# Performance work log

Hardware: AMD Instinct MI355X
Metric: run time of the kernel (lower is better)

Reference implementation:

```python
import jax, jax.numpy as jnp
import numpy as np

N = 100000   # nodes
E = 625000   # edges
D = 128      # input feature dim
H = 128      # hidden_channels
L = 2        # num_layers
NEG = 0.2    # leaky relu negative slope
BN_EPS = 1e-5


def setup_inputs() -> dict:
    key = jax.random.key(0)
    ks = jax.random.split(key, 12)
    s = 0.05
    return {
        "x": jax.random.normal(ks[0], (N, D), jnp.float32),
        "edge_index": jax.random.randint(ks[1], (2, E), 0, N, dtype=jnp.int32),
        "Wl": jax.random.normal(ks[2], (L, D, H), jnp.float32) * s,   # GATv2 lin_l (source)
        "bl": jax.random.normal(ks[3], (L, H), jnp.float32) * s,
        "Wr": jax.random.normal(ks[4], (L, D, H), jnp.float32) * s,   # GATv2 lin_r (target)
        "br": jax.random.normal(ks[5], (L, H), jnp.float32) * s,
        "att": jax.random.normal(ks[6], (L, H), jnp.float32) * s,     # attention vector a
        "cb": jax.random.normal(ks[7], (L, H), jnp.float32) * s,      # conv output bias
        "Wlin": jax.random.normal(ks[8], (L, H, H), jnp.float32) * s, # extra Linear
        "blin": jax.random.normal(ks[9], (L, H), jnp.float32) * s,
        "gamma": jnp.ones((L, H), jnp.float32),                       # BatchNorm weight
        "beta": jnp.zeros((L, H), jnp.float32),                       # BatchNorm bias
    }


def reference(x, edge_index, Wl, bl, Wr, br, att, cb, Wlin, blin, gamma, beta):
    src, dst = edge_index[0], edge_index[1]
    for i in range(L):
        # GATv2Conv (1 head, no self-loops)
        xs = x @ Wl[i] + bl[i]                 # [N, H] source transform
        xd = x @ Wr[i] + br[i]                 # [N, H] target transform
        e = jax.nn.leaky_relu(xs[src] + xd[dst], NEG)   # [E, H]
        logits = e @ att[i]                    # [E]
        m = jax.ops.segment_max(logits, dst, num_segments=N)
        a = jnp.exp(logits - m[dst])
        denom = jax.ops.segment_sum(a, dst, num_segments=N) + 1e-16
        alpha = a / denom[dst]                 # scatter-softmax over dst
        out = jax.ops.segment_sum(alpha[:, None] * xs[src], dst, num_segments=N) + cb[i]
        # x += lin(x)
        out = out + out @ Wlin[i] + blin[i]
        # BatchNorm1d (training mode: batch stats, biased var)
        mu = out.mean(axis=0)
        var = out.var(axis=0)
        x = (out - mu) * jax.lax.rsqrt(var + BN_EPS) * gamma[i] + beta[i]
        if i < L - 1:
            x = jax.nn.relu(x)
    return x
```

## Files before the change

kernel.cpp:

```cpp
#include <hip/hip_runtime.h>

#define NN 100000
#define NE 625000
#define HD 128

typedef unsigned int u32;
typedef unsigned short u16;
typedef __bf16 bf16x8 __attribute__((ext_vector_type(8)));
typedef float f32x4 __attribute__((ext_vector_type(4)));
typedef float f32x2 __attribute__((ext_vector_type(2)));

__device__ __forceinline__ u16 f2b(float f) {
  u32 u = __float_as_uint(f);
  u32 r = (u + 0x7FFFu + ((u >> 16) & 1u)) >> 16;
  return (u16)r;
}
__device__ __forceinline__ float b2f(u32 u) { return __uint_as_float(u << 16); }

template <int CTRL>
__device__ __forceinline__ float dppadd(float x) {
  int t = __builtin_amdgcn_update_dpp(0, __float_as_int(x), CTRL, 0xf, 0xf, true);
  return x + __int_as_float(t);
}

__global__ void k_prep_w(const float* __restrict__ Wl, const float* __restrict__ Wr,
                         const float* __restrict__ Wlin, u16* __restrict__ Wt) {
  int i = blockIdx.x * blockDim.x + threadIdx.x;
  if (i >= 6 * 16384) return;
  int mat = i >> 14;
  int l = mat / 3, which = mat % 3;
  int rem = i & 16383;
  int hh = rem >> 7, dd = rem & 127;
  const float* src = (which == 0) ? Wl : (which == 1) ? Wr : Wlin;
  float v = src[l * 16384 + dd * 128 + hh];
  if (which == 2 && dd == hh) v += 1.0f;
  Wt[l * (3 * 16384) + which * 16384 + hh * 128 + dd] = f2b(v);
}

__global__ void k_cast_x(const float* __restrict__ x, u16* __restrict__ xb) {
  int i = blockIdx.x * blockDim.x + threadIdx.x;
  if (i >= NN * 32) return;
  float4 v = *(const float4*)(x + i * 4);
  uint2 o;
  o.x = (u32)f2b(v.x) | ((u32)f2b(v.y) << 16);
  o.y = (u32)f2b(v.z) | ((u32)f2b(v.w) << 16);
  *(uint2*)(xb + i * 4) = o;
}

__global__ void k_hist(const int* __restrict__ dst, int* __restrict__ deg) {
  int e = blockIdx.x * blockDim.x + threadIdx.x;
  if (e < NE) atomicAdd(&deg[dst[e]], 1);
}

__global__ void k_alloc(const int* __restrict__ deg, int* __restrict__ row_start,
                        int* __restrict__ cursor) {
  int idx = blockIdx.x * blockDim.x + threadIdx.x;
  int lane = threadIdx.x & 63;
  int v = (idx < NN) ? deg[idx] : 0;
  int incl = v;
  #pragma unroll
  for (int off = 1; off < 64; off <<= 1) {
    int t = __shfl_up(incl, off, 64);
    if (lane >= off) incl += t;
  }
  int total = __shfl(incl, 63, 64);
  int base = 0;
  if (lane == 63) base = atomicAdd(cursor, total);
  base = __shfl(base, 63, 64);
  if (idx < NN) row_start[idx] = base + incl - v;
}

__global__ void k_fill(const int* __restrict__ src, const int* __restrict__ dst,
                       const int* __restrict__ row_start, int* __restrict__ cnt,
                       int* __restrict__ ss) {
  int e = blockIdx.x * blockDim.x + threadIdx.x;
  if (e >= NE) return;
  int d = dst[e];
  int p = row_start[d] + atomicAdd(&cnt[d], 1);
  ss[p] = src[e];
}

__global__ __launch_bounds__(256) void k_gemm4(
    const u16* __restrict__ A, const u16* __restrict__ Bt0, const u16* __restrict__ Bt1,
    const float* __restrict__ bias0, const float* __restrict__ bias1,
    u16* __restrict__ o0, u16* __restrict__ o1,
    const float* __restrict__ bn_sum, const float* __restrict__ bn_sq,
    const float* __restrict__ bn_g, const float* __restrict__ bn_b,
    float* __restrict__ st_sum, float* __restrict__ st_sq, int nB) {
  __shared__ __align__(16) u16 lA[128 * 136];
  __shared__ __align__(16) u16 lB[64 * 136];
  const int tid = threadIdx.x;
  const int m0 = blockIdx.x * 128;
  const int rr = tid >> 4;
  const int seg = tid & 15;

  float mu[8], sc[8], bb[8];
  if (bn_sum) {
    const float invn = 1.0f / 100000.0f;
    #pragma unroll
    for (int j = 0; j < 8; ++j) {
      int c = seg * 8 + j;
      float m = bn_sum[c] * invn;
      float v = fmaxf(bn_sq[c] * invn - m * m, 0.f);
      mu[j] = m;
      sc[j] = rsqrtf(v + 1e-5f) * bn_g[c];
      bb[j] = bn_b[c];
    }
  }
  #pragma unroll
  for (int p = 0; p < 8; ++p) {
    int row = p * 16 + rr;
    int g = m0 + row;
    int gc = (g < NN) ? g : (NN - 1);
    uint4 v = *(const uint4*)(A + gc * HD + seg * 8);
    if (bn_sum) {
      u32 w[4] = {v.x, v.y, v.z, v.w};
      #pragma unroll
      for (int k = 0; k < 4; ++k) {
        float lo = fmaxf((b2f(w[k] & 0xFFFFu) - mu[2 * k]) * sc[2 * k] + bb[2 * k], 0.f);
        float hi = fmaxf((b2f(w[k] >> 16) - mu[2 * k + 1]) * sc[2 * k + 1] + bb[2 * k + 1], 0.f);
        w[k] = (u32)f2b(lo) | ((u32)f2b(hi) << 16);
      }
      v.x = w[0]; v.y = w[1]; v.z = w[2]; v.w = w[3];
    }
    *(uint4*)(lA + row * 136 + seg * 8) = v;
  }
  #pragma unroll
  for (int p = 0; p < 4; ++p) {
    int n = p * 16 + rr;
    uint4 v = *(const uint4*)(Bt0 + n * HD + seg * 8);
    *(uint4*)(lB + n * 136 + seg * 8) = v;
  }
  __syncthreads();

  const int wv = tid >> 6;
  const int lane = tid & 63;
  const int colt = lane & 15;
  const int kq = lane >> 4;
  const int rq = kq * 4;
  bf16x8 af[2][4];
  #pragma unroll
  for (int tile = 0; tile < 2; ++tile)
    #pragma unroll
    for (int s = 0; s < 4; ++s)
      af[tile][s] = *(const bf16x8*)(lA + ((wv * 2 + tile) * 16 + colt) * 136 + s * 32 + kq * 8);

  for (int pass = 0; pass < nB; ++pass) {
    const u16* Bt = pass ? Bt1 : Bt0;
    u16* o = pass ? o1 : o0;
    const float* bias = pass ? bias1 : bias0;
    if (pass == 1) {
      __syncthreads();
      #pragma unroll
      for (int p = 0; p < 4; ++p) {
        int n = p * 16 + rr;
        uint4 v = *(const uint4*)(Bt + n * HD + seg * 8);
        *(uint4*)(lB + n * 136 + seg * 8) = v;
      }
      __syncthreads();
    }
    #pragma unroll
    for (int half = 0; half < 2; ++half) {
      if (half == 1) {
        __syncthreads();
        #pragma unroll
        for (int p = 0; p < 4; ++p) {
          int n = p * 16 + rr;
          uint4 v = *(const uint4*)(Bt + (64 + n) * HD + seg * 8);
          *(uint4*)(lB + n * 136 + seg * 8) = v;
        }
        __syncthreads();
      }
      #pragma unroll
      for (int tt = 0; tt < 4; ++tt) {
        int t = half * 4 + tt;
        bf16x8 bf[4];
        #pragma unroll
        for (int s = 0; s < 4; ++s)
          bf[s] = *(const bf16x8*)(lB + (tt * 16 + colt) * 136 + s * 32 + kq * 8);
        const int c = t * 16 + colt;
        const float bs = bias[c];
        #pragma unroll
        for (int tile = 0; tile < 2; ++tile) {
          f32x4 acc = {0.f, 0.f, 0.f, 0.f};
          #pragma unroll
          for (int s = 0; s < 4; ++s)
            acc = __builtin_amdgcn_mfma_f32_16x16x32_bf16(af[tile][s], bf[s], acc, 0, 0, 0);
          #pragma unroll
          for (int r = 0; r < 4; ++r)
            lA[((wv * 2 + tile) * 16 + rq + r) * 136 + c] = f2b(acc[r] + bs);
        }
      }
    }
    __syncthreads();
    float s8[8], q8[8];
    #pragma unroll
    for (int j = 0; j < 8; ++j) { s8[j] = 0.f; q8[j] = 0.f; }
    #pragma unroll
    for (int i = 0; i < 8; ++i) {
      int row = i * 16 + rr;
      int g = m0 + row;
      if (g < NN) {
        uint4 v = *(const uint4*)(lA + row * 136 + seg * 8);
        *(uint4*)(o + g * HD + seg * 8) = v;
        if (st_sum && pass == 0) {
          u32 w[4] = {v.x, v.y, v.z, v.w};
          #pragma unroll
          for (int k = 0; k < 4; ++k) {
            float lo = b2f(w[k] & 0xFFFFu), hi = b2f(w[k] >> 16);
            s8[2 * k] += lo; q8[2 * k] += lo * lo;
            s8[2 * k + 1] += hi; q8[2 * k + 1] += hi * hi;
          }
        }
      }
    }
    if (st_sum && pass == 0) {
      __syncthreads();
      float* red = (float*)lB;
      #pragma unroll
      for (int j = 0; j < 8; ++j) {
        red[rr * 128 + seg * 8 + j] = s8[j];
        red[2048 + rr * 128 + seg * 8 + j] = q8[j];
      }
      __syncthreads();
      if (tid < 128) {
        float S = 0.f, Q = 0.f;
        #pragma unroll
        for (int u = 0; u < 16; ++u) {
          S += red[u * 128 + tid];
          Q += red[2048 + u * 128 + tid];
        }
        atomicAdd(&st_sum[tid], S);
        atomicAdd(&st_sq[tid], Q);
      }
    }
  }
}

__global__ __launch_bounds__(256) void k_edge4(
    const u16* __restrict__ xs_b, const u16* __restrict__ xd_b,
    const int* __restrict__ row_start, const int* __restrict__ deg,
    const int* __restrict__ ss, const float* __restrict__ att,
    const float* __restrict__ cb, u16* __restrict__ out_b) {
  int dv = blockIdx.x * 4 + (threadIdx.x >> 6);
  if (dv >= NN) return;
  const int lane = threadIdx.x & 63;
  const int cl = lane & 15;
  const int grp = lane >> 4;

  const float L2E = 1.4426950408889634f;
  float4 av0 = *(const float4*)(att + cl * 8);
  float4 av1 = *(const float4*)(att + cl * 8 + 4);
  float al[8] = {av0.x, av0.y, av0.z, av0.w, av1.x, av1.y, av1.z, av1.w};
  f32x2 a6[4], a4[4];
  #pragma unroll
  for (int k = 0; k < 4; ++k) {
    a6[k].x = L2E * 0.6f * al[2 * k];     a6[k].y = L2E * 0.6f * al[2 * k + 1];
    a4[k].x = L2E * 0.4f * al[2 * k];     a4[k].y = L2E * 0.4f * al[2 * k + 1];
  }
  uint4 xdp = *(const uint4*)(xd_b + dv * HD + cl * 8);
  u32 xdw[4] = {xdp.x, xdp.y, xdp.z, xdp.w};
  f32x2 xd4[4];
  #pragma unroll
  for (int k = 0; k < 4; ++k) {
    xd4[k].x = __uint_as_float(xdw[k] << 16);
    xd4[k].y = __uint_as_float(xdw[k] & 0xFFFF0000u);
  }

  const int base = row_start[dv];
  const int n = deg[dv];
  f32x2 acc[4] = {{0.f, 0.f}, {0.f, 0.f}, {0.f, 0.f}, {0.f, 0.f}};
  float wsum = 0.f;

  for (int e0 = 0; e0 < n; e0 += 4) {
    int e = e0 + grp;
    int idx = ss[base + ((e < n) ? e : 0)];
    uint4 p = *(const uint4*)(xs_b + idx * HD + cl * 8);
    u32 pw[4] = {p.x, p.y, p.z, p.w};
    f32x2 xv[4];
    f32x2 qv = {0.f, 0.f};
    #pragma unroll
    for (int k = 0; k < 4; ++k) {
      f32x2 x2;
      x2.x = __uint_as_float(pw[k] << 16);
      x2.y = __uint_as_float(pw[k] & 0xFFFF0000u);
      xv[k] = x2;
      f32x2 t = x2 + xd4[k];
      f32x2 ab = {__builtin_fabsf(t.x), __builtin_fabsf(t.y)};
      qv += a4[k] * ab;
      qv += a6[k] * t;
    }
    float q = qv.x + qv.y;
    q = dppadd<0xB1>(q);
    q = dppadd<0x4E>(q);
    q = dppadd<0x124>(q);
    q = dppadd<0x128>(q);
    float w = (e < n) ? exp2f(q) : 0.f;
    wsum += w;
    #pragma unroll
    for (int k = 0; k < 4; ++k) acc[k] += xv[k] * w;
  }

  #pragma unroll
  for (int k = 0; k < 4; ++k) {
    acc[k].x += __shfl_xor(acc[k].x, 16, 64);
    acc[k].y += __shfl_xor(acc[k].y, 16, 64);
    acc[k].x += __shfl_xor(acc[k].x, 32, 64);
    acc[k].y += __shfl_xor(acc[k].y, 32, 64);
  }
  wsum += __shfl_xor(wsum, 16, 64);
  wsum += __shfl_xor(wsum, 32, 64);

  if (grp == 0) {
    float inv = 1.f / (wsum + 1e-16f);
    float4 cb0 = *(const float4*)(cb + cl * 8);
    float4 cb1 = *(const float4*)(cb + cl * 8 + 4);
    float cbl[8] = {cb0.x, cb0.y, cb0.z, cb0.w, cb1.x, cb1.y, cb1.z, cb1.w};
    u32 ow[4];
    #pragma unroll
    for (int k = 0; k < 4; ++k) {
      float o0 = acc[k].x * inv + cbl[2 * k];
      float o1 = acc[k].y * inv + cbl[2 * k + 1];
      ow[k] = (u32)f2b(o0) | ((u32)f2b(o1) << 16);
    }
    uint4 o;
    o.x = ow[0]; o.y = ow[1]; o.z = ow[2]; o.w = ow[3];
    *(uint4*)(out_b + dv * HD + cl * 8) = o;
  }
}

__global__ void k_bn(const u16* __restrict__ hb, const float* __restrict__ ssum,
                     const float* __restrict__ ssq, const float* __restrict__ gamma,
                     const float* __restrict__ beta, float* __restrict__ fout) {
  int i = blockIdx.x * blockDim.x + threadIdx.x;
  if (i >= NN * 64) return;
  int cp = (i & 63) * 2;
  u32 xp = ((const u32*)hb)[i];
  float v0 = b2f(xp & 0xFFFFu), v1 = b2f(xp >> 16);
  const float invn = 1.0f / 100000.0f;
  float mu0 = ssum[cp] * invn, mu1 = ssum[cp + 1] * invn;
  float va0 = fmaxf(ssq[cp] * invn - mu0 * mu0, 0.f);
  float va1 = fmaxf(ssq[cp + 1] * invn - mu1 * mu1, 0.f);
  float s0 = rsqrtf(va0 + 1e-5f) * gamma[cp];
  float s1 = rsqrtf(va1 + 1e-5f) * gamma[cp + 1];
  float o0 = (v0 - mu0) * s0 + beta[cp];
  float o1 = (v1 - mu1) * s1 + beta[cp + 1];
  int row = i >> 6;
  *(float2*)(fout + row * 128 + cp) = make_float2(o0, o1);
}

extern "C" void kernel_launch(void* const* d_in, const int* in_sizes, int n_in,
                              void* d_out, int out_size, void* d_ws, size_t ws_size,
                              hipStream_t stream) {
  const float* x    = (const float*)d_in[0];
  const int*   ei   = (const int*)d_in[1];
  const float* Wl   = (const float*)d_in[2];
  const float* bl   = (const float*)d_in[3];
  const float* Wr   = (const float*)d_in[4];
  const float* br   = (const float*)d_in[5];
  const float* att  = (const float*)d_in[6];
  const float* cb   = (const float*)d_in[7];
  const float* Wlin = (const float*)d_in[8];
  const float* blin = (const float*)d_in[9];
  const float* gm   = (const float*)d_in[10];
  const float* bt   = (const float*)d_in[11];
  const int* esrc = ei;
  const int* edst = ei + NE;

  u16* xb    = (u16*)d_ws;
  u16* xs_b  = xb + NN * HD;
  u16* xd_b  = xs_b + NN * HD;
  u16* out_b = xd_b + NN * HD;
  u16* Wt    = out_b + NN * HD;
  int* deg       = (int*)(Wt + 6 * 16384);
  int* cnt       = deg + NN;
  int* cursor    = cnt + NN;
  int* row_start = cursor + 1;
  int* srcs      = row_start + NN;
  float* ssum0   = (float*)(srcs + NE);
  float* ssq0    = ssum0 + 128;
  float* ssum1   = ssq0 + 128;
  float* ssq1    = ssum1 + 128;

  hipMemsetAsync(deg, 0, (size_t)(2 * NN + 1) * 4, stream);
  hipMemsetAsync(ssum0, 0, 4 * 128 * 4, stream);
  k_prep_w<<<(6 * 16384 + 255) / 256, 256, 0, stream>>>(Wl, Wr, Wlin, Wt);
  k_cast_x<<<(NN * 32 + 255) / 256, 256, 0, stream>>>(x, xb);
  k_hist<<<(NE + 255) / 256, 256, 0, stream>>>(edst, deg);
  k_alloc<<<(NN + 255) / 256, 256, 0, stream>>>(deg, row_start, cursor);
  k_fill<<<(NE + 255) / 256, 256, 0, stream>>>(esrc, edst, row_start, cnt, srcs);

  const int gg = (NN + 127) / 128;
  const u16* wt0_l = Wt;             const u16* wt0_r = Wt + 16384;     const u16* wt0_lin = Wt + 2 * 16384;
  const u16* wt1_l = Wt + 3 * 16384; const u16* wt1_r = Wt + 4 * 16384; const u16* wt1_lin = Wt + 5 * 16384;

  k_gemm4<<<gg, 256, 0, stream>>>(xb, wt0_l, wt0_r, bl, br, xs_b, xd_b,
                                  nullptr, nullptr, nullptr, nullptr,
                                  nullptr, nullptr, 2);
  k_edge4<<<(NN + 3) / 4, 256, 0, stream>>>(xs_b, xd_b, row_start, deg, srcs,
                                            att, cb, out_b);
  k_gemm4<<<gg, 256, 0, stream>>>(out_b, wt0_lin, nullptr, blin, nullptr,
                                  out_b, nullptr,
                                  nullptr, nullptr, nullptr, nullptr,
                                  ssum0, ssq0, 1);
  k_gemm4<<<gg, 256, 0, stream>>>(out_b, wt1_l, wt1_r, bl + 128, br + 128,
                                  xs_b, xd_b,
                                  ssum0, ssq0, gm, bt,
                                  nullptr, nullptr, 2);
  k_edge4<<<(NN + 3) / 4, 256, 0, stream>>>(xs_b, xd_b, row_start, deg, srcs,
                                            att + 128, cb + 128, out_b);
  k_gemm4<<<gg, 256, 0, stream>>>(out_b, wt1_lin, nullptr, blin + 128, nullptr,
                                  out_b, nullptr,
                                  nullptr, nullptr, nullptr, nullptr,
                                  ssum1, ssq1, 1);
  k_bn<<<(NN * 64 + 255) / 256, 256, 0, stream>>>(out_b, ssum1, ssq1,
                                                  gm + 128, bt + 128, (float*)d_out);
}
```

Measured before the change: 457.4 us.

## Persistent edge kernel with software-pipelined double-buffered neighbor gathers

The edge aggregation kernel becomes a persistent grid-stride kernel with 2048 blocks. Each wavefront loops over many destination nodes and hoists the att/cb loads out of that loop. Within a node, the first 32 neighbors are gathered two chunks ahead of the compute that uses them, so multiple xs row loads are in flight and gather latency is hidden. Index loads read four consecutive entries and select per group, which relies on 32 zero-padded entries after srcs to stay in bounds. The cost is more registers and an unrolled code path, plus more branching.

```diff
diff --git a/kernel.cpp b/kernel.cpp
--- a/kernel.cpp
+++ b/kernel.cpp
@@ -237,16 +237,16 @@
   }
 }
 
-__global__ __launch_bounds__(256) void k_edge4(
+__global__ __launch_bounds__(256) void k_edge5(
     const u16* __restrict__ xs_b, const u16* __restrict__ xd_b,
     const int* __restrict__ row_start, const int* __restrict__ deg,
     const int* __restrict__ ss, const float* __restrict__ att,
     const float* __restrict__ cb, u16* __restrict__ out_b) {
-  int dv = blockIdx.x * 4 + (threadIdx.x >> 6);
-  if (dv >= NN) return;
   const int lane = threadIdx.x & 63;
   const int cl = lane & 15;
   const int grp = lane >> 4;
+  const int nw = gridDim.x * 4;
+  const int wid = blockIdx.x * 4 + (threadIdx.x >> 6);
 
   const float L2E = 1.4426950408889634f;
   float4 av0 = *(const float4*)(att + cl * 8);
@@ -258,74 +258,105 @@
     a6[k].x = L2E * 0.6f * al[2 * k];     a6[k].y = L2E * 0.6f * al[2 * k + 1];
     a4[k].x = L2E * 0.4f * al[2 * k];     a4[k].y = L2E * 0.4f * al[2 * k + 1];
   }
-  uint4 xdp = *(const uint4*)(xd_b + dv * HD + cl * 8);
-  u32 xdw[4] = {xdp.x, xdp.y, xdp.z, xdp.w};
-  f32x2 xd4[4];
-  #pragma unroll
-  for (int k = 0; k < 4; ++k) {
-    xd4[k].x = __uint_as_float(xdw[k] << 16);
-    xd4[k].y = __uint_as_float(xdw[k] & 0xFFFF0000u);
-  }
-
-  const int base = row_start[dv];
-  const int n = deg[dv];
-  f32x2 acc[4] = {{0.f, 0.f}, {0.f, 0.f}, {0.f, 0.f}, {0.f, 0.f}};
-  float wsum = 0.f;
-
-  for (int e0 = 0; e0 < n; e0 += 4) {
-    int e = e0 + grp;
-    int idx = ss[base + ((e < n) ? e : 0)];
-    uint4 p = *(const uint4*)(xs_b + idx * HD + cl * 8);
-    u32 pw[4] = {p.x, p.y, p.z, p.w};
-    f32x2 xv[4];
-    f32x2 qv = {0.f, 0.f};
+  float4 cb0 = *(const float4*)(cb + cl * 8);
+  float4 cb1 = *(const float4*)(cb + cl * 8 + 4);
+  float cbl[8] = {cb0.x, cb0.y, cb0.z, cb0.w, cb1.x, cb1.y, cb1.z, cb1.w};
+
+  const bool g1 = (grp & 1), g2 = (grp & 2);
+
+  for (int dv = wid; dv < NN; dv += nw) {
+    const int base = __builtin_amdgcn_readfirstlane(row_start[dv]);
+    const int n = __builtin_amdgcn_readfirstlane(deg[dv]);
+    const int* sp = ss + base;
+
+    uint4 xdp = *(const uint4*)(xd_b + (size_t)dv * HD + cl * 8);
+    u32 xdw[4] = {xdp.x, xdp.y, xdp.z, xdp.w};
+    f32x2 xd4[4];
     #pragma unroll
     for (int k = 0; k < 4; ++k) {
-      f32x2 x2;
-      x2.x = __uint_as_float(pw[k] << 16);
-      x2.y = __uint_as_float(pw[k] & 0xFFFF0000u);
-      xv[k] = x2;
-      f32x2 t = x2 + xd4[k];
-      f32x2 ab = {__builtin_fabsf(t.x), __builtin_fabsf(t.y)};
-      qv += a4[k] * ab;
-      qv += a6[k] * t;
-    }
-    float q = qv.x + qv.y;
-    q = dppadd<0xB1>(q);
-    q = dppadd<0x4E>(q);
-    q = dppadd<0x124>(q);
-    q = dppadd<0x128>(q);
-    float w = (e < n) ? exp2f(q) : 0.f;
-    wsum += w;
-    #pragma unroll
-    for (int k = 0; k < 4; ++k) acc[k] += xv[k] * w;
-  }
-
-  #pragma unroll
-  for (int k = 0; k < 4; ++k) {
-    acc[k].x += __shfl_xor(acc[k].x, 16, 64);
-    acc[k].y += __shfl_xor(acc[k].y, 16, 64);
-    acc[k].x += __shfl_xor(acc[k].x, 32, 64);
-    acc[k].y += __shfl_xor(acc[k].y, 32, 64);
-  }
-  wsum += __shfl_xor(wsum, 16, 64);
-  wsum += __shfl_xor(wsum, 32, 64);
-
-  if (grp == 0) {
-    float inv = 1.f / (wsum + 1e-16f);
-    float4 cb0 = *(const float4*)(cb + cl * 8);
-    float4 cb1 = *(const float4*)(cb + cl * 8 + 4);
-    float cbl[8] = {cb0.x, cb0.y, cb0.z, cb0.w, cb1.x, cb1.y, cb1.z, cb1.w};
-    u32 ow[4];
+      xd4[k].x = __uint_as_float(xdw[k] << 16);
+      xd4[k].y = __uint_as_float(xdw[k] & 0xFFFF0000u);
+    }
+
+    f32x2 acc[4] = {{0.f, 0.f}, {0.f, 0.f}, {0.f, 0.f}, {0.f, 0.f}};
+    float wsum = 0.f;
+
+    auto GATH = [&](int j) -> uint4 {
+      int a = sp[4 * j], b = sp[4 * j + 1], c = sp[4 * j + 2], d = sp[4 * j + 3];
+      int ia = g1 ? b : a;
+      int ib = g1 ? d : c;
+      u32 ix = (u32)(g2 ? ib : ia);
+      ix = (ix < (u32)NN) ? ix : 0u;
+      return *(const uint4*)(xs_b + (size_t)ix * HD + cl * 8);
+    };
+    auto COMP = [&](int j, uint4 p) {
+      u32 pw[4] = {p.x, p.y, p.z, p.w};
+      f32x2 xv[4];
+      f32x2 qv = {0.f, 0.f};
+      #pragma unroll
+      for (int k = 0; k < 4; ++k) {
+        f32x2 x2;
+        x2.x = __uint_as_float(pw[k] << 16);
+        x2.y = __uint_as_float(pw[k] & 0xFFFF0000u);
+        xv[k] = x2;
+        f32x2 t = x2 + xd4[k];
+        f32x2 ab = {__builtin_fabsf(t.x), __builtin_fabsf(t.y)};
+        qv += a4[k] * ab;
+        qv += a6[k] * t;
+      }
+      float q = qv.x + qv.y;
+      q = dppadd<0xB1>(q);
+      q = dppadd<0x4E>(q);
+      q = dppadd<0x124>(q);
+      q = dppadd<0x128>(q);
+      float w = (4 * j + grp < n) ? exp2f(q) : 0.f;
+      wsum += w;
+      #pragma unroll
+      for (int k = 0; k < 4; ++k) acc[k] += xv[k] * w;
+    };
+
+    uint4 pA, pB;
+    if (n > 0)  pA = GATH(0);
+    if (n > 4)  pB = GATH(1);
+    if (n > 0)  { COMP(0, pA); if (n > 8)  pA = GATH(2); }
+    if (n > 4)  { COMP(1, pB); if (n > 12) pB = GATH(3); }
+    if (n > 8)  { COMP(2, pA); if (n > 16) pA = GATH(4); }
+    if (n > 12) { COMP(3, pB); if (n > 20) pB = GATH(5); }
+    if (n > 16) { COMP(4, pA); if (n > 24) pA = GATH(6); }
+    if (n > 20) { COMP(5, pB); if (n > 28) pB = GATH(7); }
+    if (n > 24) COMP(6, pA);
+    if (n > 28) COMP(7, pB);
+    for (int e0 = 32; e0 < n; e0 += 4) {
+      int e = e0 + grp;
+      int ixl = sp[(e < n) ? e : 0];
+      u32 ix = ((u32)ixl < (u32)NN) ? (u32)ixl : 0u;
+      uint4 p = *(const uint4*)(xs_b + (size_t)ix * HD + cl * 8);
+      COMP(e0 >> 2, p);
+    }
+
     #pragma unroll
     for (int k = 0; k < 4; ++k) {
-      float o0 = acc[k].x * inv + cbl[2 * k];
-      float o1 = acc[k].y * inv + cbl[2 * k + 1];
-      ow[k] = (u32)f2b(o0) | ((u32)f2b(o1) << 16);
-    }
-    uint4 o;
-    o.x = ow[0]; o.y = ow[1]; o.z = ow[2]; o.w = ow[3];
-    *(uint4*)(out_b + dv * HD + cl * 8) = o;
+      acc[k].x += __shfl_xor(acc[k].x, 16, 64);
+      acc[k].y += __shfl_xor(acc[k].y, 16, 64);
+      acc[k].x += __shfl_xor(acc[k].x, 32, 64);
+      acc[k].y += __shfl_xor(acc[k].y, 32, 64);
+    }
+    wsum += __shfl_xor(wsum, 16, 64);
+    wsum += __shfl_xor(wsum, 32, 64);
+
+    if (grp == 0) {
+      float inv = 1.f / (wsum + 1e-16f);
+      u32 ow[4];
+      #pragma unroll
+      for (int k = 0; k < 4; ++k) {
+        float o0 = acc[k].x * inv + cbl[2 * k];
+        float o1 = acc[k].y * inv + cbl[2 * k + 1];
+        ow[k] = (u32)f2b(o0) | ((u32)f2b(o1) << 16);
+      }
+      uint4 o;
+      o.x = ow[0]; o.y = ow[1]; o.z = ow[2]; o.w = ow[3];
+      *(uint4*)(out_b + (size_t)dv * HD + cl * 8) = o;
+    }
   }
 }
 
@@ -377,12 +408,13 @@
   int* cursor    = cnt + NN;
   int* row_start = cursor + 1;
   int* srcs      = row_start + NN;
-  float* ssum0   = (float*)(srcs + NE);
+  float* ssum0   = (float*)(srcs + NE + 32);
   float* ssq0    = ssum0 + 128;
   float* ssum1   = ssq0 + 128;
   float* ssq1    = ssum1 + 128;
 
   hipMemsetAsync(deg, 0, (size_t)(2 * NN + 1) * 4, stream);
+  hipMemsetAsync(srcs + NE, 0, 32 * 4, stream);
   hipMemsetAsync(ssum0, 0, 4 * 128 * 4, stream);
   k_prep_w<<<(6 * 16384 + 255) / 256, 256, 0, stream>>>(Wl, Wr, Wlin, Wt);
   k_cast_x<<<(NN * 32 + 255) / 256, 256, 0, stream>>>(x, xb);
@@ -391,14 +423,15 @@
   k_fill<<<(NE + 255) / 256, 256, 0, stream>>>(esrc, edst, row_start, cnt, srcs);
 
   const int gg = (NN + 127) / 128;
+  const int ge = 2048;
   const u16* wt0_l = Wt;             const u16* wt0_r = Wt + 16384;     const u16* wt0_lin = Wt + 2 * 16384;
   const u16* wt1_l = Wt + 3 * 16384; const u16* wt1_r = Wt + 4 * 16384; const u16* wt1_lin = Wt + 5 * 16384;
 
   k_gemm4<<<gg, 256, 0, stream>>>(xb, wt0_l, wt0_r, bl, br, xs_b, xd_b,
                                   nullptr, nullptr, nullptr, nullptr,
                                   nullptr, nullptr, 2);
-  k_edge4<<<(NN + 3) / 4, 256, 0, stream>>>(xs_b, xd_b, row_start, deg, srcs,
-                                            att, cb, out_b);
+  k_edge5<<<ge, 256, 0, stream>>>(xs_b, xd_b, row_start, deg, srcs,
+                                  att, cb, out_b);
   k_gemm4<<<gg, 256, 0, stream>>>(out_b, wt0_lin, nullptr, blin, nullptr,
                                   out_b, nullptr,
                                   nullptr, nullptr, nullptr, nullptr,
@@ -407,8 +440,8 @@
                                   xs_b, xd_b,
                                   ssum0, ssq0, gm, bt,
                                   nullptr, nullptr, 2);
-  k_edge4<<<(NN + 3) / 4, 256, 0, stream>>>(xs_b, xd_b, row_start, deg, srcs,
-                                            att + 128, cb + 128, out_b);
+  k_edge5<<<ge, 256, 0, stream>>>(xs_b, xd_b, row_start, deg, srcs,
+                                  att + 128, cb + 128, out_b);
   k_gemm4<<<gg, 256, 0, stream>>>(out_b, wt1_lin, nullptr, blin + 128, nullptr,
                                   out_b, nullptr,
                                   nullptr, nullptr, nullptr, nullptr,
```

Result: no change. 463.1 us (+1.2%).

## Fuse fp32-to-bf16 input cast into GEMM and prefetch weight tiles into registers

Applied to the files above, without the earlier changes.

The separate k_cast_x kernel is removed. The first GEMM now reads fp32 x directly and converts it to bf16 while staging the tile into LDS, which saves one kernel launch and a full write and reread of a bf16 copy of x. All A-row and B-tile global loads are also issued up front into registers. The second weight matrix is prefetched during the first pass, so the LDS refill in the second pass no longer waits on global memory. This raises register pressure and may lower occupancy.

```diff
diff --git a/kernel.cpp b/kernel.cpp
--- a/kernel.cpp
+++ b/kernel.cpp
@@ -37,16 +37,6 @@
   Wt[l * (3 * 16384) + which * 16384 + hh * 128 + dd] = f2b(v);
 }
 
-__global__ void k_cast_x(const float* __restrict__ x, u16* __restrict__ xb) {
-  int i = blockIdx.x * blockDim.x + threadIdx.x;
-  if (i >= NN * 32) return;
-  float4 v = *(const float4*)(x + i * 4);
-  uint2 o;
-  o.x = (u32)f2b(v.x) | ((u32)f2b(v.y) << 16);
-  o.y = (u32)f2b(v.z) | ((u32)f2b(v.w) << 16);
-  *(uint2*)(xb + i * 4) = o;
-}
-
 __global__ void k_hist(const int* __restrict__ dst, int* __restrict__ deg) {
   int e = blockIdx.x * blockDim.x + threadIdx.x;
   if (e < NE) atomicAdd(&deg[dst[e]], 1);
@@ -80,8 +70,9 @@
   ss[p] = src[e];
 }
 
-__global__ __launch_bounds__(256) void k_gemm4(
-    const u16* __restrict__ A, const u16* __restrict__ Bt0, const u16* __restrict__ Bt1,
+__global__ __launch_bounds__(256) void k_gemm5(
+    const u16* __restrict__ A, const float* __restrict__ A32,
+    const u16* __restrict__ Bt0, const u16* __restrict__ Bt1,
     const float* __restrict__ bias0, const float* __restrict__ bias1,
     u16* __restrict__ o0, u16* __restrict__ o1,
     const float* __restrict__ bn_sum, const float* __restrict__ bn_sq,
@@ -107,12 +98,41 @@
       bb[j] = bn_b[c];
     }
   }
+
+  uint4 va[8];
+  float4 va32a[8], va32b[8];
+  #pragma unroll
+  for (int p = 0; p < 8; ++p) {
+    int g = m0 + p * 16 + rr;
+    int gc = (g < NN) ? g : (NN - 1);
+    if (A32) {
+      va32a[p] = *(const float4*)(A32 + (size_t)gc * HD + seg * 8);
+      va32b[p] = *(const float4*)(A32 + (size_t)gc * HD + seg * 8 + 4);
+    } else {
+      va[p] = *(const uint4*)(A + (size_t)gc * HD + seg * 8);
+    }
+  }
+  uint4 vb0[4], vb1[4];
+  #pragma unroll
+  for (int p = 0; p < 4; ++p)
+    vb0[p] = *(const uint4*)(Bt0 + (p * 16 + rr) * HD + seg * 8);
+  #pragma unroll
+  for (int p = 0; p < 4; ++p)
+    vb1[p] = *(const uint4*)(Bt0 + (64 + p * 16 + rr) * HD + seg * 8);
+
   #pragma unroll
   for (int p = 0; p < 8; ++p) {
     int row = p * 16 + rr;
-    int g = m0 + row;
-    int gc = (g < NN) ? g : (NN - 1);
-    uint4 v = *(const uint4*)(A + gc * HD + seg * 8);
+    uint4 v;
+    if (A32) {
+      float4 f0 = va32a[p], f1 = va32b[p];
+      v.x = (u32)f2b(f0.x) | ((u32)f2b(f0.y) << 16);
+      v.y = (u32)f2b(f0.z) | ((u32)f2b(f0.w) << 16);
+      v.z = (u32)f2b(f1.x) | ((u32)f2b(f1.y) << 16);
+      v.w = (u32)f2b(f1.z) | ((u32)f2b(f1.w) << 16);
+    } else {
+      v = va[p];
+    }
     if (bn_sum) {
       u32 w[4] = {v.x, v.y, v.z, v.w};
       #pragma unroll
@@ -126,11 +146,8 @@
     *(uint4*)(lA + row * 136 + seg * 8) = v;
   }
   #pragma unroll
-  for (int p = 0; p < 4; ++p) {
-    int n = p * 16 + rr;
-    uint4 v = *(const uint4*)(Bt0 + n * HD + seg * 8);
-    *(uint4*)(lB + n * 136 + seg * 8) = v;
-  }
+  for (int p = 0; p < 4; ++p)
+    *(uint4*)(lB + (p * 16 + rr) * 136 + seg * 8) = vb0[p];
   __syncthreads();
 
   const int wv = tid >> 6;
@@ -145,18 +162,15 @@
     for (int s = 0; s < 4; ++s)
       af[tile][s] = *(const bf16x8*)(lA + ((wv * 2 + tile) * 16 + colt) * 136 + s * 32 + kq * 8);
 
+  uint4 nb0[4], nb1[4];
+
   for (int pass = 0; pass < nB; ++pass) {
-    const u16* Bt = pass ? Bt1 : Bt0;
     u16* o = pass ? o1 : o0;
     const float* bias = pass ? bias1 : bias0;
     if (pass == 1) {
-      __syncthreads();
       #pragma unroll
-      for (int p = 0; p < 4; ++p) {
-        int n = p * 16 + rr;
-        uint4 v = *(const uint4*)(Bt + n * HD + seg * 8);
-        *(uint4*)(lB + n * 136 + seg * 8) = v;
-      }
+      for (int p = 0; p < 4; ++p)
+        *(uint4*)(lB + (p * 16 + rr) * 136 + seg * 8) = nb0[p];
       __syncthreads();
     }
     #pragma unroll
@@ -164,10 +178,15 @@
       if (half == 1) {
         __syncthreads();
         #pragma unroll
-        for (int p = 0; p < 4; ++p) {
-          int n = p * 16 + rr;
-          uint4 v = *(const uint4*)(Bt + (64 + n) * HD + seg * 8);
-          *(uint4*)(lB + n * 136 + seg * 8) = v;
+        for (int p = 0; p < 4; ++p)
+          *(uint4*)(lB + (p * 16 + rr) * 136 + seg * 8) = pass ? nb1[p] : vb1[p];
+        if (pass == 0 && nB == 2) {
+          #pragma unroll
+          for (int p = 0; p < 4; ++p)
+            nb0[p] = *(const uint4*)(Bt1 + (p * 16 + rr) * HD + seg * 8);
+          #pragma unroll
+          for (int p = 0; p < 4; ++p)
+            nb1[p] = *(const uint4*)(Bt1 + (64 + p * 16 + rr) * HD + seg * 8);
         }
         __syncthreads();
       }
@@ -202,7 +221,7 @@
       int g = m0 + row;
       if (g < NN) {
         uint4 v = *(const uint4*)(lA + row * 136 + seg * 8);
-        *(uint4*)(o + g * HD + seg * 8) = v;
+        *(uint4*)(o + (size_t)g * HD + seg * 8) = v;
         if (st_sum && pass == 0) {
           u32 w[4] = {v.x, v.y, v.z, v.w};
           #pragma unroll
@@ -258,7 +277,7 @@
     a6[k].x = L2E * 0.6f * al[2 * k];     a6[k].y = L2E * 0.6f * al[2 * k + 1];
     a4[k].x = L2E * 0.4f * al[2 * k];     a4[k].y = L2E * 0.4f * al[2 * k + 1];
   }
-  uint4 xdp = *(const uint4*)(xd_b + dv * HD + cl * 8);
+  uint4 xdp = *(const uint4*)(xd_b + (size_t)dv * HD + cl * 8);
   u32 xdw[4] = {xdp.x, xdp.y, xdp.z, xdp.w};
   f32x2 xd4[4];
   #pragma unroll
@@ -275,7 +294,7 @@
   for (int e0 = 0; e0 < n; e0 += 4) {
     int e = e0 + grp;
     int idx = ss[base + ((e < n) ? e : 0)];
-    uint4 p = *(const uint4*)(xs_b + idx * HD + cl * 8);
+    uint4 p = *(const uint4*)(xs_b + (size_t)idx * HD + cl * 8);
     u32 pw[4] = {p.x, p.y, p.z, p.w};
     f32x2 xv[4];
     f32x2 qv = {0.f, 0.f};
@@ -325,7 +344,7 @@
     }
     uint4 o;
     o.x = ow[0]; o.y = ow[1]; o.z = ow[2]; o.w = ow[3];
-    *(uint4*)(out_b + dv * HD + cl * 8) = o;
+    *(uint4*)(out_b + (size_t)dv * HD + cl * 8) = o;
   }
 }
 
@@ -367,8 +386,7 @@
   const int* esrc = ei;
   const int* edst = ei + NE;
 
-  u16* xb    = (u16*)d_ws;
-  u16* xs_b  = xb + NN * HD;
+  u16* xs_b  = (u16*)d_ws;
   u16* xd_b  = xs_b + NN * HD;
   u16* out_b = xd_b + NN * HD;
   u16* Wt    = out_b + NN * HD;
@@ -385,7 +403,6 @@
   hipMemsetAsync(deg, 0, (size_t)(2 * NN + 1) * 4, stream);
   hipMemsetAsync(ssum0, 0, 4 * 128 * 4, stream);
   k_prep_w<<<(6 * 16384 + 255) / 256, 256, 0, stream>>>(Wl, Wr, Wlin, Wt);
-  k_cast_x<<<(NN * 32 + 255) / 256, 256, 0, stream>>>(x, xb);
   k_hist<<<(NE + 255) / 256, 256, 0, stream>>>(edst, deg);
   k_alloc<<<(NN + 255) / 256, 256, 0, stream>>>(deg, row_start, cursor);
   k_fill<<<(NE + 255) / 256, 256, 0, stream>>>(esrc, edst, row_start, cnt, srcs);
@@ -394,22 +411,22 @@
   const u16* wt0_l = Wt;             const u16* wt0_r = Wt + 16384;     const u16* wt0_lin = Wt + 2 * 16384;
   const u16* wt1_l = Wt + 3 * 16384; const u16* wt1_r = Wt + 4 * 16384; const u16* wt1_lin = Wt + 5 * 16384;
 
-  k_gemm4<<<gg, 256, 0, stream>>>(xb, wt0_l, wt0_r, bl, br, xs_b, xd_b,
+  k_gemm5<<<gg, 256, 0, stream>>>(nullptr, x, wt0_l, wt0_r, bl, br, xs_b, xd_b,
                                   nullptr, nullptr, nullptr, nullptr,
                                   nullptr, nullptr, 2);
   k_edge4<<<(NN + 3) / 4, 256, 0, stream>>>(xs_b, xd_b, row_start, deg, srcs,
                                             att, cb, out_b);
-  k_gemm4<<<gg, 256, 0, stream>>>(out_b, wt0_lin, nullptr, blin, nullptr,
+  k_gemm5<<<gg, 256, 0, stream>>>(out_b, nullptr, wt0_lin, nullptr, blin, nullptr,
                                   out_b, nullptr,
                                   nullptr, nullptr, nullptr, nullptr,
                                   ssum0, ssq0, 1);
-  k_gemm4<<<gg, 256, 0, stream>>>(out_b, wt1_l, wt1_r, bl + 128, br + 128,
+  k_gemm5<<<gg, 256, 0, stream>>>(out_b, nullptr, wt1_l, wt1_r, bl + 128, br + 128,
                                   xs_b, xd_b,
                                   ssum0, ssq0, gm, bt,
                                   nullptr, nullptr, 2);
   k_edge4<<<(NN + 3) / 4, 256, 0, stream>>>(xs_b, xd_b, row_start, deg, srcs,
                                             att + 128, cb + 128, out_b);
-  k_gemm4<<<gg, 256, 0, stream>>>(out_b, wt1_lin, nullptr, blin + 128, nullptr,
+  k_gemm5<<<gg, 256, 0, stream>>>(out_b, nullptr, wt1_lin, nullptr, blin + 128, nullptr,
                                   out_b, nullptr,
                                   nullptr, nullptr, nullptr, nullptr,
                                   ssum1, ssq1, 1);
```

Result: slower. 474.2 us (+3.7%).

## Fuse Wlin GEMM and BatchNorm statistics into the edge aggregation kernel

Applied to the files above, without the earlier changes.

The edge-softmax aggregation kernel now handles 16 destination nodes per block, with each wave processing 4 nodes in sequence. It stages the aggregated rows in LDS and applies the Wlin projection with MFMA directly. It also computes the per-column sum and sum-of-squares there and adds them to the BatchNorm accumulators with atomics. This removes a separate GEMM launch per layer and one full write and read of the intermediate node features. The cost is far more blocks issuing atomics to the same 256 stat addresses, and less parallelism across nodes inside each block.

```diff
diff --git a/kernel.cpp b/kernel.cpp
--- a/kernel.cpp
+++ b/kernel.cpp
@@ -85,8 +85,7 @@
     const float* __restrict__ bias0, const float* __restrict__ bias1,
     u16* __restrict__ o0, u16* __restrict__ o1,
     const float* __restrict__ bn_sum, const float* __restrict__ bn_sq,
-    const float* __restrict__ bn_g, const float* __restrict__ bn_b,
-    float* __restrict__ st_sum, float* __restrict__ st_sq, int nB) {
+    const float* __restrict__ bn_g, const float* __restrict__ bn_b, int nB) {
   __shared__ __align__(16) u16 lA[128 * 136];
   __shared__ __align__(16) u16 lB[64 * 136];
   const int tid = threadIdx.x;
@@ -112,7 +111,7 @@
     int row = p * 16 + rr;
     int g = m0 + row;
     int gc = (g < NN) ? g : (NN - 1);
-    uint4 v = *(const uint4*)(A + gc * HD + seg * 8);
+    uint4 v = *(const uint4*)(A + (size_t)gc * HD + seg * 8);
     if (bn_sum) {
       u32 w[4] = {v.x, v.y, v.z, v.w};
       #pragma unroll
@@ -193,58 +192,31 @@
       }
     }
     __syncthreads();
-    float s8[8], q8[8];
-    #pragma unroll
-    for (int j = 0; j < 8; ++j) { s8[j] = 0.f; q8[j] = 0.f; }
     #pragma unroll
     for (int i = 0; i < 8; ++i) {
       int row = i * 16 + rr;
       int g = m0 + row;
       if (g < NN) {
         uint4 v = *(const uint4*)(lA + row * 136 + seg * 8);
-        *(uint4*)(o + g * HD + seg * 8) = v;
-        if (st_sum && pass == 0) {
-          u32 w[4] = {v.x, v.y, v.z, v.w};
-          #pragma unroll
-          for (int k = 0; k < 4; ++k) {
-            float lo = b2f(w[k] & 0xFFFFu), hi = b2f(w[k] >> 16);
-            s8[2 * k] += lo; q8[2 * k] += lo * lo;
-            s8[2 * k + 1] += hi; q8[2 * k + 1] += hi * hi;
-          }
-        }
-      }
-    }
-    if (st_sum && pass == 0) {
-      __syncthreads();
-      float* red = (float*)lB;
-      #pragma unroll
-      for (int j = 0; j < 8; ++j) {
-        red[rr * 128 + seg * 8 + j] = s8[j];
-        red[2048 + rr * 128 + seg * 8 + j] = q8[j];
-      }
-      __syncthreads();
-      if (tid < 128) {
-        float S = 0.f, Q = 0.f;
-        #pragma unroll
-        for (int u = 0; u < 16; ++u) {
-          S += red[u * 128 + tid];
-          Q += red[2048 + u * 128 + tid];
-        }
-        atomicAdd(&st_sum[tid], S);
-        atomicAdd(&st_sq[tid], Q);
-      }
-    }
-  }
-}
-
-__global__ __launch_bounds__(256) void k_edge4(
+        *(uint4*)(o + (size_t)g * HD + seg * 8) = v;
+      }
+    }
+  }
+}
+
+__global__ __launch_bounds__(256) void k_edge6(
     const u16* __restrict__ xs_b, const u16* __restrict__ xd_b,
     const int* __restrict__ row_start, const int* __restrict__ deg,
     const int* __restrict__ ss, const float* __restrict__ att,
-    const float* __restrict__ cb, u16* __restrict__ out_b) {
-  int dv = blockIdx.x * 4 + (threadIdx.x >> 6);
-  if (dv >= NN) return;
-  const int lane = threadIdx.x & 63;
+    const float* __restrict__ cb, const u16* __restrict__ WlinT,
+    const float* __restrict__ blin, u16* __restrict__ out_b,
+    float* __restrict__ st_sum, float* __restrict__ st_sq) {
+  __shared__ __align__(16) u16 lT[16 * 136];
+  __shared__ __align__(16) u16 lO[16 * 136];
+  __shared__ float red[4096];
+  const int tid = threadIdx.x;
+  const int wv = tid >> 6;
+  const int lane = tid & 63;
   const int cl = lane & 15;
   const int grp = lane >> 4;
 
@@ -258,74 +230,127 @@
     a6[k].x = L2E * 0.6f * al[2 * k];     a6[k].y = L2E * 0.6f * al[2 * k + 1];
     a4[k].x = L2E * 0.4f * al[2 * k];     a4[k].y = L2E * 0.4f * al[2 * k + 1];
   }
-  uint4 xdp = *(const uint4*)(xd_b + dv * HD + cl * 8);
-  u32 xdw[4] = {xdp.x, xdp.y, xdp.z, xdp.w};
-  f32x2 xd4[4];
+  float4 cb0 = *(const float4*)(cb + cl * 8);
+  float4 cb1 = *(const float4*)(cb + cl * 8 + 4);
+  float cbl[8] = {cb0.x, cb0.y, cb0.z, cb0.w, cb1.x, cb1.y, cb1.z, cb1.w};
+
+  #pragma unroll 1
+  for (int it = 0; it < 4; ++it) {
+    const int dv = blockIdx.x * 16 + wv * 4 + it;
+    uint4 xdp = *(const uint4*)(xd_b + (size_t)dv * HD + cl * 8);
+    u32 xdw[4] = {xdp.x, xdp.y, xdp.z, xdp.w};
+    f32x2 xd4[4];
+    #pragma unroll
+    for (int k = 0; k < 4; ++k) {
+      xd4[k].x = __uint_as_float(xdw[k] << 16);
+      xd4[k].y = __uint_as_float(xdw[k] & 0xFFFF0000u);
+    }
+    const int base = row_start[dv];
+    const int n = deg[dv];
+    f32x2 acc[4] = {{0.f, 0.f}, {0.f, 0.f}, {0.f, 0.f}, {0.f, 0.f}};
+    float wsum = 0.f;
+
+    for (int e0 = 0; e0 < n; e0 += 4) {
+      int e = e0 + grp;
+      int idx = ss[base + ((e < n) ? e : 0)];
+      uint4 p = *(const uint4*)(xs_b + (size_t)idx * HD + cl * 8);
+      u32 pw[4] = {p.x, p.y, p.z, p.w};
+      f32x2 xv[4];
+      f32x2 qv = {0.f, 0.f};
+      #pragma unroll
+      for (int k = 0; k < 4; ++k) {
+        f32x2 x2;
+        x2.x = __uint_as_float(pw[k] << 16);
+        x2.y = __uint_as_float(pw[k] & 0xFFFF0000u);
+        xv[k] = x2;
+        f32x2 t = x2 + xd4[k];
+        f32x2 ab = {__builtin_fabsf(t.x), __builtin_fabsf(t.y)};
+        qv += a4[k] * ab;
+        qv += a6[k] * t;
+      }
+      float q = qv.x + qv.y;
+      q = dppadd<0xB1>(q);
+      q = dppadd<0x4E>(q);
+      q = dppadd<0x124>(q);
+      q = dppadd<0x128>(q);
+      float w = (e < n) ? exp2f(q) : 0.f;
+      wsum += w;
+      #pragma unroll
+      for (int k = 0; k < 4; ++k) acc[k] += xv[k] * w;
+    }
+
+    #pragma unroll
+    for (int k = 0; k < 4; ++k) {
+      acc[k].x += __shfl_xor(acc[k].x, 16, 64);
+      acc[k].y += __shfl_xor(acc[k].y, 16, 64);
+      acc[k].x += __shfl_xor(acc[k].x, 32, 64);
+      acc[k].y += __shfl_xor(acc[k].y, 32, 64);
+    }
+    wsum += __shfl_xor(wsum, 16, 64);
+    wsum += __shfl_xor(wsum, 32, 64);
+
+    if (grp == 0) {
+      float inv = 1.f / (wsum + 1e-16f);
+      u32 ow[4];
+      #pragma unroll
+      for (int k = 0; k < 4; ++k) {
+        float o0 = acc[k].x * inv + cbl[2 * k];
+        float o1 = acc[k].y * inv + cbl[2 * k + 1];
+        ow[k] = (u32)f2b(o0) | ((u32)f2b(o1) << 16);
+      }
+      uint4 o;
+      o.x = ow[0]; o.y = ow[1]; o.z = ow[2]; o.w = ow[3];
+      *(uint4*)(lT + (wv * 4 + it) * 136 + cl * 8) = o;
+    }
+  }
+  __syncthreads();
+
+  {
+    bf16x8 af[4];
+    #pragma unroll
+    for (int s = 0; s < 4; ++s)
+      af[s] = *(const bf16x8*)(lT + cl * 136 + s * 32 + grp * 8);
+    #pragma unroll
+    for (int t2 = 0; t2 < 2; ++t2) {
+      int tt = wv * 2 + t2;
+      const u16* Bb = WlinT + (tt * 16 + cl) * HD + grp * 8;
+      bf16x8 bf[4];
+      #pragma unroll
+      for (int s = 0; s < 4; ++s) bf[s] = *(const bf16x8*)(Bb + s * 32);
+      f32x4 acc = {0.f, 0.f, 0.f, 0.f};
+      #pragma unroll
+      for (int s = 0; s < 4; ++s)
+        acc = __builtin_amdgcn_mfma_f32_16x16x32_bf16(af[s], bf[s], acc, 0, 0, 0);
+      const float bs = blin[tt * 16 + cl];
+      #pragma unroll
+      for (int r = 0; r < 4; ++r)
+        lO[(grp * 4 + r) * 136 + tt * 16 + cl] = f2b(acc[r] + bs);
+    }
+  }
+  __syncthreads();
+
+  const int row = tid >> 4, seg = tid & 15;
+  uint4 v = *(const uint4*)(lO + row * 136 + seg * 8);
+  *(uint4*)(out_b + ((size_t)blockIdx.x * 16 + row) * HD + seg * 8) = v;
+  u32 w[4] = {v.x, v.y, v.z, v.w};
   #pragma unroll
   for (int k = 0; k < 4; ++k) {
-    xd4[k].x = __uint_as_float(xdw[k] << 16);
-    xd4[k].y = __uint_as_float(xdw[k] & 0xFFFF0000u);
-  }
-
-  const int base = row_start[dv];
-  const int n = deg[dv];
-  f32x2 acc[4] = {{0.f, 0.f}, {0.f, 0.f}, {0.f, 0.f}, {0.f, 0.f}};
-  float wsum = 0.f;
-
-  for (int e0 = 0; e0 < n; e0 += 4) {
-    int e = e0 + grp;
-    int idx = ss[base + ((e < n) ? e : 0)];
-    uint4 p = *(const uint4*)(xs_b + idx * HD + cl * 8);
-    u32 pw[4] = {p.x, p.y, p.z, p.w};
-    f32x2 xv[4];
-    f32x2 qv = {0.f, 0.f};
-    #pragma unroll
-    for (int k = 0; k < 4; ++k) {
-      f32x2 x2;
-      x2.x = __uint_as_float(pw[k] << 16);
-      x2.y = __uint_as_float(pw[k] & 0xFFFF0000u);
-      xv[k] = x2;
-      f32x2 t = x2 + xd4[k];
-      f32x2 ab = {__builtin_fabsf(t.x), __builtin_fabsf(t.y)};
-      qv += a4[k] * ab;
-      qv += a6[k] * t;
-    }
-    float q = qv.x + qv.y;
-    q = dppadd<0xB1>(q);
-    q = dppadd<0x4E>(q);
-    q = dppadd<0x124>(q);
-    q = dppadd<0x128>(q);
-    float w = (e < n) ? exp2f(q) : 0.f;
-    wsum += w;
-    #pragma unroll
-    for (int k = 0; k < 4; ++k) acc[k] += xv[k] * w;
-  }
-
-  #pragma unroll
-  for (int k = 0; k < 4; ++k) {
-    acc[k].x += __shfl_xor(acc[k].x, 16, 64);
-    acc[k].y += __shfl_xor(acc[k].y, 16, 64);
-    acc[k].x += __shfl_xor(acc[k].x, 32, 64);
-    acc[k].y += __shfl_xor(acc[k].y, 32, 64);
-  }
-  wsum += __shfl_xor(wsum, 16, 64);
-  wsum += __shfl_xor(wsum, 32, 64);
-
-  if (grp == 0) {
-    float inv = 1.f / (wsum + 1e-16f);
-    float4 cb0 = *(const float4*)(cb + cl * 8);
-    float4 cb1 = *(const float4*)(cb + cl * 8 + 4);
-    float cbl[8] = {cb0.x, cb0.y, cb0.z, cb0.w, cb1.x, cb1.y, cb1.z, cb1.w};
-    u32 ow[4];
-    #pragma unroll
-    for (int k = 0; k < 4; ++k) {
-      float o0 = acc[k].x * inv + cbl[2 * k];
-      float o1 = acc[k].y * inv + cbl[2 * k + 1];
-      ow[k] = (u32)f2b(o0) | ((u32)f2b(o1) << 16);
-    }
-    uint4 o;
-    o.x = ow[0]; o.y = ow[1]; o.z = ow[2]; o.w = ow[3];
-    *(uint4*)(out_b + dv * HD + cl * 8) = o;
+    float lo = b2f(w[k] & 0xFFFFu), hi = b2f(w[k] >> 16);
+    red[row * 128 + seg * 8 + 2 * k] = lo;
+    red[row * 128 + seg * 8 + 2 * k + 1] = hi;
+    red[2048 + row * 128 + seg * 8 + 2 * k] = lo * lo;
+    red[2048 + row * 128 + seg * 8 + 2 * k + 1] = hi * hi;
+  }
+  __syncthreads();
+  if (tid < 128) {
+    float S = 0.f, Q = 0.f;
+    #pragma unroll
+    for (int u = 0; u < 16; ++u) {
+      S += red[u * 128 + tid];
+      Q += red[2048 + u * 128 + tid];
+    }
+    atomicAdd(&st_sum[tid], S);
+    atomicAdd(&st_sq[tid], Q);
   }
 }
 
@@ -391,28 +416,20 @@
   k_fill<<<(NE + 255) / 256, 256, 0, stream>>>(esrc, edst, row_start, cnt, srcs);
 
   const int gg = (NN + 127) / 128;
+  const int ge = NN / 16;
   const u16* wt0_l = Wt;             const u16* wt0_r = Wt + 16384;     const u16* wt0_lin = Wt + 2 * 16384;
   const u16* wt1_l = Wt + 3 * 16384; const u16* wt1_r = Wt + 4 * 16384; const u16* wt1_lin = Wt + 5 * 16384;
 
   k_gemm4<<<gg, 256, 0, stream>>>(xb, wt0_l, wt0_r, bl, br, xs_b, xd_b,
-                                  nullptr, nullptr, nullptr, nullptr,
-                                  nullptr, nullptr, 2);
-  k_edge4<<<(NN + 3) / 4, 256, 0, stream>>>(xs_b, xd_b, row_start, deg, srcs,
-                                            att, cb, out_b);
-  k_gemm4<<<gg, 256, 0, stream>>>(out_b, wt0_lin, nullptr, blin, nullptr,
-                                  out_b, nullptr,
-                                  nullptr, nullptr, nullptr, nullptr,
-                                  ssum0, ssq0, 1);
+                                  nullptr, nullptr, nullptr, nullptr, 2);
+  k_edge6<<<ge, 256, 0, stream>>>(xs_b, xd_b, row_start, deg, srcs,
+                                  att, cb, wt0_lin, blin, out_b, ssum0, ssq0);
   k_gemm4<<<gg, 256, 0, stream>>>(out_b, wt1_l, wt1_r, bl + 128, br + 128,
                                   xs_b, xd_b,
-                                  ssum0, ssq0, gm, bt,
-                                  nullptr, nullptr, 2);
-  k_edge4<<<(NN + 3) / 4, 256, 0, stream>>>(xs_b, xd_b, row_start, deg, srcs,
-                                            att + 128, cb + 128, out_b);
-  k_gemm4<<<gg, 256, 0, stream>>>(out_b, wt1_lin, nullptr, blin + 128, nullptr,
-                                  out_b, nullptr,
-                                  nullptr, nullptr, nullptr, nullptr,
-                                  ssum1, ssq1, 1);
+                                  ssum0, ssq0, gm, bt, 2);
+  k_edge6<<<ge, 256, 0, stream>>>(xs_b, xd_b, row_start, deg, srcs,
+                                  att + 128, cb + 128, wt1_lin, blin + 128,
+                                  out_b, ssum1, ssq1);
   k_bn<<<(NN * 64 + 255) / 256, 256, 0, stream>>>(out_b, ssum1, ssq1,
                                                   gm + 128, bt + 128, (float*)d_out);
 }
```

New measurement: 715.8 us. +56.5%, slower.
